# Optimization experiments

Measured on AMD Instinct MI355X. Metric: run time of the kernel, lower is better.

Reference implementation:

```python
import jax, jax.numpy as jnp
import numpy as np

N_QUBITS = 12          # log2(input_num)
DIM = 1 << N_QUBITS    # 4096
BATCH = 4096
OUTPUT_NUM = 10


def setup_inputs() -> dict:
    key = jax.random.key(0)
    k1, k2 = jax.random.split(key)
    x = jax.random.normal(k1, (BATCH, DIM), dtype=jnp.float32)
    # normalized statevectors (amplitude encoding), as a VQC expects
    x = x / jnp.linalg.norm(x, axis=1, keepdims=True)
    theta = jax.random.normal(k2, (2 * N_QUBITS,), dtype=jnp.float32) * jnp.pi
    return {"x": x, "theta": theta}


def _ry(theta):
    # [[cos(t/2), -sin(t/2)], [sin(t/2), cos(t/2)]]
    c, s = jnp.cos(theta / 2), jnp.sin(theta / 2)
    return jnp.stack([jnp.stack([c, -s]), jnp.stack([s, c])]).astype(jnp.complex64)


def _apply_1q(state, U, q, n):
    # state: [2^n, B]; qubit q is bit q of the row index (qubit 0 = LSB,
    # matching the kron ordering temp = kron(gate_i, temp) in the original).
    B = state.shape[1]
    hi = 1 << (n - 1 - q)
    lo = 1 << q
    s = state.reshape(hi, 2, lo * B)
    s = jnp.einsum('ab,xby->xay', U, s)
    return s.reshape(1 << n, B)


def _cz_phase(n):
    # vqc_10 applies CZ on adjacent pairs (n-2-i, n-1-i) for i in 0..n-2,
    # then CZ(0, n-1). CZ is diagonal; the swap sandwiches cancel exactly.
    idx = jnp.arange(1 << n)
    pairs = [(i, i + 1) for i in range(n - 1)] + [(0, n - 1)]
    par = jnp.zeros_like(idx)
    for p, q in pairs:
        par = par + ((idx >> p) & 1) * ((idx >> q) & 1)
    return jnp.where(par % 2 == 1, -1.0, 1.0).astype(jnp.complex64)


def reference(x, theta):
    n = N_QUBITS
    state = x.T.astype(jnp.complex64)            # [2^n, B]
    # first RY layer, thetas[0:n], theta[i] on qubit i
    for q in range(n):
        state = _apply_1q(state, _ry(theta[q]), q, n)
    # CZ entangling layer (diagonal)
    state = state * _cz_phase(n)[:, None]
    # second RY layer, thetas[n:2n]
    for q in range(n):
        state = _apply_1q(state, _ry(theta[n + q]), q, n)
    # measurement: P(qubit k == 1) for the first OUTPUT_NUM qubits
    probs = state.real ** 2 + state.imag ** 2    # [2^n, B]
    idx = jnp.arange(DIM)
    bits = ((idx[:, None] >> jnp.arange(OUTPUT_NUM)[None, :]) & 1).astype(probs.dtype)  # [2^n, K]
    out = jnp.einsum('db,dk->bk', probs, bits)   # [B, OUTPUT_NUM]
    return out
```

## Files before the change

kernel.cpp:

```cpp
#include <hip/hip_runtime.h>
#include <math.h>

#define DIM  4096
#define KOUT 10
#define BATCH 4096

typedef float float2v __attribute__((ext_vector_type(2)));

__device__ __forceinline__ int swzAddr(int lin) {
    return lin ^ (((lin >> 6) & 7) << 2);
}

__device__ __forceinline__ float rlane(float v, int lane) {
    return __int_as_float(__builtin_amdgcn_readlane(__float_as_int(v), lane));
}

__device__ __forceinline__ void ldsFence() {
    __builtin_amdgcn_sched_barrier(0);
    asm volatile("s_waitcnt lgkmcnt(0)" ::: "memory");
    __builtin_amdgcn_sched_barrier(0);
}

template<int KP>
__device__ __forceinline__ void liftPk(float2v r2[32], float t, float s) {
    const float2v tv = { -t, -t };
    const float2v sv = {  s,  s };
#pragma unroll
    for (int m = 0; m < 16; ++m) {
        const int i0 = ((m >> KP) << (KP + 1)) | (m & ((1 << KP) - 1));
        const int i1 = i0 | (1 << KP);
        float2v a = r2[i0], b = r2[i1];
        float2v a1 = __builtin_elementwise_fma(tv, b, a);
        float2v b1 = __builtin_elementwise_fma(sv, a1, b);
        r2[i1] = b1;
        r2[i0] = __builtin_elementwise_fma(tv, b1, a1);
    }
}

__device__ __forceinline__ void liftIntra(float2v r2[32], float t, float s) {
#pragma unroll
    for (int m = 0; m < 32; ++m) {
        float a = r2[m].x, b = r2[m].y;
        float a1 = fmaf(-t, b, a);
        float b1 = fmaf(s, a1, b);
        r2[m].x = fmaf(-t, b1, a1);
        r2[m].y = b1;
    }
}

__device__ __forceinline__ void transpose64(float2v r2[32], float* lds, int l) {
    float tmp[32];
    ldsFence();
    if (l < 32) {
#pragma unroll
        for (int e4 = 0; e4 < 16; ++e4)
            *reinterpret_cast<float4*>(&lds[swzAddr(l * 64 + e4 * 4)]) =
                make_float4(r2[2 * e4].x, r2[2 * e4].y,
                            r2[2 * e4 + 1].x, r2[2 * e4 + 1].y);
    }
#pragma unroll
    for (int j = 0; j < 32; ++j)
        tmp[j] = lds[swzAddr(j * 64 + l)];
    ldsFence();
    if (l >= 32) {
#pragma unroll
        for (int e4 = 0; e4 < 16; ++e4)
            *reinterpret_cast<float4*>(&lds[swzAddr((l - 32) * 64 + e4 * 4)]) =
                make_float4(r2[2 * e4].x, r2[2 * e4].y,
                            r2[2 * e4 + 1].x, r2[2 * e4 + 1].y);
    }
#pragma unroll
    for (int m = 0; m < 16; ++m) {
        float2v w;
        w.x = lds[swzAddr((2 * m) * 64 + l)];
        w.y = lds[swzAddr((2 * m + 1) * 64 + l)];
        r2[16 + m] = w;
    }
#pragma unroll
    for (int m = 0; m < 16; ++m) {
        float2v w; w.x = tmp[2 * m]; w.y = tmp[2 * m + 1];
        r2[m] = w;
    }
}

__global__ __launch_bounds__(64) void vqc_kernel(
        const float* __restrict__ x,
        const float* __restrict__ theta,
        float* __restrict__ out)
{
    __shared__ __align__(16) float lds[2048];
    const int l = threadIdx.x;
    const int b = blockIdx.x;

    float th = theta[l < 24 ? l : 0];
    float qh = 0.25f * th;
    float sq = sinf(qh), cq = cosf(qh);
    float sfull = 2.f * sq * cq;
    float tt, ss;
    if (fabsf(sq) <= fabsf(cq)) { tt = sq / cq;  ss = sfull;  }
    else                        { tt = -cq / sq; ss = -sfull; }

    float2v r2[32];
    const float4* x4 = reinterpret_cast<const float4*>(x + (size_t)b * DIM + l * 64);
#pragma unroll
    for (int e4 = 0; e4 < 16; ++e4) {
        const float4 w = x4[e4];
        float2v lo; lo.x = w.x; lo.y = w.y;
        float2v hi; hi.x = w.z; hi.y = w.w;
        r2[2 * e4]     = lo;
        r2[2 * e4 + 1] = hi;
    }

    liftIntra (r2, rlane(tt, 0), rlane(ss, 0));
    liftPk<0>(r2, rlane(tt, 1), rlane(ss, 1));
    liftPk<1>(r2, rlane(tt, 2), rlane(ss, 2));
    liftPk<2>(r2, rlane(tt, 3), rlane(ss, 3));
    liftPk<3>(r2, rlane(tt, 4), rlane(ss, 4));
    liftPk<4>(r2, rlane(tt, 5), rlane(ss, 5));

    transpose64(r2, lds, l);

    liftIntra (r2, rlane(tt, 6),  rlane(ss, 6));
    liftPk<0>(r2, rlane(tt, 7),  rlane(ss, 7));
    liftPk<1>(r2, rlane(tt, 8),  rlane(ss, 8));
    liftPk<2>(r2, rlane(tt, 9),  rlane(ss, 9));
    liftPk<3>(r2, rlane(tt, 10), rlane(ss, 10));
    liftPk<4>(r2, rlane(tt, 11), rlane(ss, 11));

    {
        int f  = __popc(l & (l >> 1) & 0x1F) & 1;
        int l5 = (l >> 5) & 1, l0 = l & 1;
        float sg0 = f              ? -1.f : 1.f;
        float sg1 = (f ^ l5)       ? -1.f : 1.f;
        float sg2 = (f ^ l0)       ? -1.f : 1.f;
        float sg3 = (f ^ l5 ^ l0)  ? -1.f : 1.f;
#pragma unroll
        for (int e = 0; e < 64; ++e) {
            const int Ce  = __popc(e & (e >> 1) & 0x1F) & 1;
            const int sel = (e & 1) | (((e >> 5) & 1) << 1);
            float sgn;
            if      (sel == 0) sgn = sg0;
            else if (sel == 1) sgn = sg1;
            else if (sel == 2) sgn = sg2;
            else               sgn = sg3;
            const float m = Ce ? -sgn : sgn;
            if (e & 1) r2[e >> 1].y *= m;
            else       r2[e >> 1].x *= m;
        }
    }

    liftIntra (r2, rlane(tt, 18), rlane(ss, 18));
    liftPk<0>(r2, rlane(tt, 19), rlane(ss, 19));
    liftPk<1>(r2, rlane(tt, 20), rlane(ss, 20));
    liftPk<2>(r2, rlane(tt, 21), rlane(ss, 21));
    liftPk<3>(r2, rlane(tt, 22), rlane(ss, 22));
    liftPk<4>(r2, rlane(tt, 23), rlane(ss, 23));

    transpose64(r2, lds, l);

    liftIntra (r2, rlane(tt, 12), rlane(ss, 12));
    liftPk<0>(r2, rlane(tt, 13), rlane(ss, 13));
    liftPk<1>(r2, rlane(tt, 14), rlane(ss, 14));
    liftPk<2>(r2, rlane(tt, 15), rlane(ss, 15));
    liftPk<3>(r2, rlane(tt, 16), rlane(ss, 16));
    liftPk<4>(r2, rlane(tt, 17), rlane(ss, 17));

#pragma unroll
    for (int m = 0; m < 32; ++m) r2[m] *= r2[m];

    float v0 = 0.f, v1 = 0.f, v2 = 0.f, v3 = 0.f, v4 = 0.f;
    float q32[32];
#pragma unroll
    for (int m = 0; m < 32; ++m) { v0 += r2[m].y; q32[m] = r2[m].x + r2[m].y; }
    float q16[16];
#pragma unroll
    for (int m = 0; m < 16; ++m) { v1 += q32[2*m+1]; q16[m] = q32[2*m] + q32[2*m+1]; }
    float q8[8];
#pragma unroll
    for (int m = 0; m < 8; ++m)  { v2 += q16[2*m+1]; q8[m] = q16[2*m] + q16[2*m+1]; }
    float q4[4];
#pragma unroll
    for (int m = 0; m < 4; ++m)  { v3 += q8[2*m+1]; q4[m] = q8[2*m] + q8[2*m+1]; }
    float q2[2];
#pragma unroll
    for (int m = 0; m < 2; ++m)  { v4 += q4[2*m+1]; q2[m] = q4[2*m] + q4[2*m+1]; }
    const float v5   = q2[1];
    const float psum = q2[0] + q2[1];

    float v[10];
    v[0] = v0; v[1] = v1; v[2] = v2; v[3] = v3; v[4] = v4; v[5] = v5;
    v[6] = (l & 1) ? psum : 0.f;
    v[7] = (l & 2) ? psum : 0.f;
    v[8] = (l & 4) ? psum : 0.f;
    v[9] = (l & 8) ? psum : 0.f;

#pragma unroll
    for (int k = 0; k < 10; ++k) {
        float t = v[k];
#pragma unroll
        for (int off = 32; off >= 1; off >>= 1)
            t += __shfl_xor(t, off, 64);
        v[k] = t;
    }

    if (l == 0) {
#pragma unroll
        for (int k = 0; k < KOUT; ++k) out[b * KOUT + k] = v[k];
    }
}

extern "C" void kernel_launch(void* const* d_in, const int* in_sizes, int n_in,
                              void* d_out, int out_size, void* d_ws, size_t ws_size,
                              hipStream_t stream) {
    const float* x     = (const float*)d_in[0];
    const float* theta = (const float*)d_in[1];
    float* out         = (float*)d_out;
    vqc_kernel<<<BATCH, 64, 0, stream>>>(x, theta, out);
}
```

Measured before the change: 27.31 us.

## Process two batch rows per wavefront to interleave independent work

Each 64-thread block now handles two statevectors (rows b and b+2048), interleaving their gate lifts, transposes and reductions so two independent dependency chains can hide each other's latency. The grid is halved to 2048 blocks, LDS per block doubles, and theta, sign and shuffle costs are amortised over two rows. In exchange, register use roughly doubles, which lowers occupancy or risks spills, and the smaller grid exposes fewer waves for latency hiding.

Result: slower. 31.99 us (+17.1%).

```diff
diff --git a/kernel.cpp b/kernel.cpp
--- a/kernel.cpp
+++ b/kernel.cpp
@@ -4,6 +4,7 @@
 #define DIM  4096
 #define KOUT 10
 #define BATCH 4096
+#define NBLK 2048
 
 typedef float float2v __attribute__((ext_vector_type(2)));
 
@@ -48,49 +49,83 @@
     }
 }
 
-__device__ __forceinline__ void transpose64(float2v r2[32], float* lds, int l) {
-    float tmp[32];
+__device__ __forceinline__ void writeRow(float* lds, int row, const float2v* r2) {
+#pragma unroll
+    for (int e4 = 0; e4 < 16; ++e4)
+        *reinterpret_cast<float4*>(&lds[swzAddr(row * 64 + e4 * 4)]) =
+            make_float4(r2[2 * e4].x, r2[2 * e4].y,
+                        r2[2 * e4 + 1].x, r2[2 * e4 + 1].y);
+}
+
+__device__ __forceinline__ void transposePair(float2v rA[32], float2v rB[32],
+                                              float* ldsA, float* ldsB, int l) {
+    float tA[32], tB[32];
     ldsFence();
-    if (l < 32) {
-#pragma unroll
-        for (int e4 = 0; e4 < 16; ++e4)
-            *reinterpret_cast<float4*>(&lds[swzAddr(l * 64 + e4 * 4)]) =
-                make_float4(r2[2 * e4].x, r2[2 * e4].y,
-                            r2[2 * e4 + 1].x, r2[2 * e4 + 1].y);
-    }
-#pragma unroll
-    for (int j = 0; j < 32; ++j)
-        tmp[j] = lds[swzAddr(j * 64 + l)];
+    if (l < 32) { writeRow(ldsA, l, rA); writeRow(ldsB, l, rB); }
+#pragma unroll
+    for (int j = 0; j < 32; ++j) tA[j] = ldsA[swzAddr(j * 64 + l)];
+#pragma unroll
+    for (int j = 0; j < 32; ++j) tB[j] = ldsB[swzAddr(j * 64 + l)];
     ldsFence();
-    if (l >= 32) {
-#pragma unroll
-        for (int e4 = 0; e4 < 16; ++e4)
-            *reinterpret_cast<float4*>(&lds[swzAddr((l - 32) * 64 + e4 * 4)]) =
-                make_float4(r2[2 * e4].x, r2[2 * e4].y,
-                            r2[2 * e4 + 1].x, r2[2 * e4 + 1].y);
-    }
+    if (l >= 32) { writeRow(ldsA, l - 32, rA); writeRow(ldsB, l - 32, rB); }
 #pragma unroll
     for (int m = 0; m < 16; ++m) {
         float2v w;
-        w.x = lds[swzAddr((2 * m) * 64 + l)];
-        w.y = lds[swzAddr((2 * m + 1) * 64 + l)];
-        r2[16 + m] = w;
+        w.x = ldsA[swzAddr((2 * m) * 64 + l)];
+        w.y = ldsA[swzAddr((2 * m + 1) * 64 + l)];
+        rA[16 + m] = w;
     }
 #pragma unroll
     for (int m = 0; m < 16; ++m) {
-        float2v w; w.x = tmp[2 * m]; w.y = tmp[2 * m + 1];
-        r2[m] = w;
-    }
-}
-
-__global__ __launch_bounds__(64) void vqc_kernel(
+        float2v w;
+        w.x = ldsB[swzAddr((2 * m) * 64 + l)];
+        w.y = ldsB[swzAddr((2 * m + 1) * 64 + l)];
+        rB[16 + m] = w;
+    }
+#pragma unroll
+    for (int m = 0; m < 16; ++m) { float2v w; w.x = tA[2*m]; w.y = tA[2*m+1]; rA[m] = w; }
+#pragma unroll
+    for (int m = 0; m < 16; ++m) { float2v w; w.x = tB[2*m]; w.y = tB[2*m+1]; rB[m] = w; }
+}
+
+__device__ __forceinline__ void measure(float2v r2[32], int l, float v[10]) {
+#pragma unroll
+    for (int m = 0; m < 32; ++m) r2[m] *= r2[m];
+    float v0 = 0.f, v1 = 0.f, v2 = 0.f, v3 = 0.f, v4 = 0.f;
+    float q32[32];
+#pragma unroll
+    for (int m = 0; m < 32; ++m) { v0 += r2[m].y; q32[m] = r2[m].x + r2[m].y; }
+    float q16[16];
+#pragma unroll
+    for (int m = 0; m < 16; ++m) { v1 += q32[2*m+1]; q16[m] = q32[2*m] + q32[2*m+1]; }
+    float q8[8];
+#pragma unroll
+    for (int m = 0; m < 8; ++m)  { v2 += q16[2*m+1]; q8[m] = q16[2*m] + q16[2*m+1]; }
+    float q4[4];
+#pragma unroll
+    for (int m = 0; m < 4; ++m)  { v3 += q8[2*m+1]; q4[m] = q8[2*m] + q8[2*m+1]; }
+    float q2[2];
+#pragma unroll
+    for (int m = 0; m < 2; ++m)  { v4 += q4[2*m+1]; q2[m] = q4[2*m] + q4[2*m+1]; }
+    const float v5   = q2[1];
+    const float psum = q2[0] + q2[1];
+    v[0] = v0; v[1] = v1; v[2] = v2; v[3] = v3; v[4] = v4; v[5] = v5;
+    v[6] = (l & 1) ? psum : 0.f;
+    v[7] = (l & 2) ? psum : 0.f;
+    v[8] = (l & 4) ? psum : 0.f;
+    v[9] = (l & 8) ? psum : 0.f;
+}
+
+__global__ __launch_bounds__(64, 2) void vqc_kernel(
         const float* __restrict__ x,
         const float* __restrict__ theta,
         float* __restrict__ out)
 {
-    __shared__ __align__(16) float lds[2048];
+    __shared__ __align__(16) float lds[2 * 2048];
     const int l = threadIdx.x;
     const int b = blockIdx.x;
+    float* ldsA = lds;
+    float* ldsB = lds + 2048;
 
     float th = theta[l < 24 ? l : 0];
     float qh = 0.25f * th;
@@ -100,32 +135,39 @@
     if (fabsf(sq) <= fabsf(cq)) { tt = sq / cq;  ss = sfull;  }
     else                        { tt = -cq / sq; ss = -sfull; }
 
-    float2v r2[32];
-    const float4* x4 = reinterpret_cast<const float4*>(x + (size_t)b * DIM + l * 64);
+    float2v rA[32], rB[32];
+    const float4* xA = reinterpret_cast<const float4*>(x + (size_t)b * DIM + l * 64);
+    const float4* xB = reinterpret_cast<const float4*>(x + (size_t)(b + NBLK) * DIM + l * 64);
 #pragma unroll
     for (int e4 = 0; e4 < 16; ++e4) {
-        const float4 w = x4[e4];
+        const float4 w = xA[e4];
         float2v lo; lo.x = w.x; lo.y = w.y;
         float2v hi; hi.x = w.z; hi.y = w.w;
-        r2[2 * e4]     = lo;
-        r2[2 * e4 + 1] = hi;
-    }
-
-    liftIntra (r2, rlane(tt, 0), rlane(ss, 0));
-    liftPk<0>(r2, rlane(tt, 1), rlane(ss, 1));
-    liftPk<1>(r2, rlane(tt, 2), rlane(ss, 2));
-    liftPk<2>(r2, rlane(tt, 3), rlane(ss, 3));
-    liftPk<3>(r2, rlane(tt, 4), rlane(ss, 4));
-    liftPk<4>(r2, rlane(tt, 5), rlane(ss, 5));
-
-    transpose64(r2, lds, l);
-
-    liftIntra (r2, rlane(tt, 6),  rlane(ss, 6));
-    liftPk<0>(r2, rlane(tt, 7),  rlane(ss, 7));
-    liftPk<1>(r2, rlane(tt, 8),  rlane(ss, 8));
-    liftPk<2>(r2, rlane(tt, 9),  rlane(ss, 9));
-    liftPk<3>(r2, rlane(tt, 10), rlane(ss, 10));
-    liftPk<4>(r2, rlane(tt, 11), rlane(ss, 11));
+        rA[2 * e4] = lo; rA[2 * e4 + 1] = hi;
+    }
+#pragma unroll
+    for (int e4 = 0; e4 < 16; ++e4) {
+        const float4 w = xB[e4];
+        float2v lo; lo.x = w.x; lo.y = w.y;
+        float2v hi; hi.x = w.z; hi.y = w.w;
+        rB[2 * e4] = lo; rB[2 * e4 + 1] = hi;
+    }
+
+    liftIntra (rA, rlane(tt, 0), rlane(ss, 0));  liftIntra (rB, rlane(tt, 0), rlane(ss, 0));
+    liftPk<0>(rA, rlane(tt, 1), rlane(ss, 1));   liftPk<0>(rB, rlane(tt, 1), rlane(ss, 1));
+    liftPk<1>(rA, rlane(tt, 2), rlane(ss, 2));   liftPk<1>(rB, rlane(tt, 2), rlane(ss, 2));
+    liftPk<2>(rA, rlane(tt, 3), rlane(ss, 3));   liftPk<2>(rB, rlane(tt, 3), rlane(ss, 3));
+    liftPk<3>(rA, rlane(tt, 4), rlane(ss, 4));   liftPk<3>(rB, rlane(tt, 4), rlane(ss, 4));
+    liftPk<4>(rA, rlane(tt, 5), rlane(ss, 5));   liftPk<4>(rB, rlane(tt, 5), rlane(ss, 5));
+
+    transposePair(rA, rB, ldsA, ldsB, l);
+
+    liftIntra (rA, rlane(tt, 6),  rlane(ss, 6));  liftIntra (rB, rlane(tt, 6),  rlane(ss, 6));
+    liftPk<0>(rA, rlane(tt, 7),  rlane(ss, 7));   liftPk<0>(rB, rlane(tt, 7),  rlane(ss, 7));
+    liftPk<1>(rA, rlane(tt, 8),  rlane(ss, 8));   liftPk<1>(rB, rlane(tt, 8),  rlane(ss, 8));
+    liftPk<2>(rA, rlane(tt, 9),  rlane(ss, 9));   liftPk<2>(rB, rlane(tt, 9),  rlane(ss, 9));
+    liftPk<3>(rA, rlane(tt, 10), rlane(ss, 10));  liftPk<3>(rB, rlane(tt, 10), rlane(ss, 10));
+    liftPk<4>(rA, rlane(tt, 11), rlane(ss, 11));  liftPk<4>(rB, rlane(tt, 11), rlane(ss, 11));
 
     {
         int f  = __popc(l & (l >> 1) & 0x1F) & 1;
@@ -144,68 +186,48 @@
             else if (sel == 2) sgn = sg2;
             else               sgn = sg3;
             const float m = Ce ? -sgn : sgn;
-            if (e & 1) r2[e >> 1].y *= m;
-            else       r2[e >> 1].x *= m;
+            if (e & 1) { rA[e >> 1].y *= m; rB[e >> 1].y *= m; }
+            else       { rA[e >> 1].x *= m; rB[e >> 1].x *= m; }
         }
     }
 
-    liftIntra (r2, rlane(tt, 18), rlane(ss, 18));
-    liftPk<0>(r2, rlane(tt, 19), rlane(ss, 19));
-    liftPk<1>(r2, rlane(tt, 20), rlane(ss, 20));
-    liftPk<2>(r2, rlane(tt, 21), rlane(ss, 21));
-    liftPk<3>(r2, rlane(tt, 22), rlane(ss, 22));
-    liftPk<4>(r2, rlane(tt, 23), rlane(ss, 23));
-
-    transpose64(r2, lds, l);
-
-    liftIntra (r2, rlane(tt, 12), rlane(ss, 12));
-    liftPk<0>(r2, rlane(tt, 13), rlane(ss, 13));
-    liftPk<1>(r2, rlane(tt, 14), rlane(ss, 14));
-    liftPk<2>(r2, rlane(tt, 15), rlane(ss, 15));
-    liftPk<3>(r2, rlane(tt, 16), rlane(ss, 16));
-    liftPk<4>(r2, rlane(tt, 17), rlane(ss, 17));
-
-#pragma unroll
-    for (int m = 0; m < 32; ++m) r2[m] *= r2[m];
-
-    float v0 = 0.f, v1 = 0.f, v2 = 0.f, v3 = 0.f, v4 = 0.f;
-    float q32[32];
-#pragma unroll
-    for (int m = 0; m < 32; ++m) { v0 += r2[m].y; q32[m] = r2[m].x + r2[m].y; }
-    float q16[16];
-#pragma unroll
-    for (int m = 0; m < 16; ++m) { v1 += q32[2*m+1]; q16[m] = q32[2*m] + q32[2*m+1]; }
-    float q8[8];
-#pragma unroll
-    for (int m = 0; m < 8; ++m)  { v2 += q16[2*m+1]; q8[m] = q16[2*m] + q16[2*m+1]; }
-    float q4[4];
-#pragma unroll
-    for (int m = 0; m < 4; ++m)  { v3 += q8[2*m+1]; q4[m] = q8[2*m] + q8[2*m+1]; }
-    float q2[2];
-#pragma unroll
-    for (int m = 0; m < 2; ++m)  { v4 += q4[2*m+1]; q2[m] = q4[2*m] + q4[2*m+1]; }
-    const float v5   = q2[1];
-    const float psum = q2[0] + q2[1];
-
-    float v[10];
-    v[0] = v0; v[1] = v1; v[2] = v2; v[3] = v3; v[4] = v4; v[5] = v5;
-    v[6] = (l & 1) ? psum : 0.f;
-    v[7] = (l & 2) ? psum : 0.f;
-    v[8] = (l & 4) ? psum : 0.f;
-    v[9] = (l & 8) ? psum : 0.f;
-
-#pragma unroll
-    for (int k = 0; k < 10; ++k) {
-        float t = v[k];
-#pragma unroll
-        for (int off = 32; off >= 1; off >>= 1)
-            t += __shfl_xor(t, off, 64);
-        v[k] = t;
+    liftIntra (rA, rlane(tt, 18), rlane(ss, 18)); liftIntra (rB, rlane(tt, 18), rlane(ss, 18));
+    liftPk<0>(rA, rlane(tt, 19), rlane(ss, 19));  liftPk<0>(rB, rlane(tt, 19), rlane(ss, 19));
+    liftPk<1>(rA, rlane(tt, 20), rlane(ss, 20));  liftPk<1>(rB, rlane(tt, 20), rlane(ss, 20));
+    liftPk<2>(rA, rlane(tt, 21), rlane(ss, 21));  liftPk<2>(rB, rlane(tt, 21), rlane(ss, 21));
+    liftPk<3>(rA, rlane(tt, 22), rlane(ss, 22));  liftPk<3>(rB, rlane(tt, 22), rlane(ss, 22));
+    liftPk<4>(rA, rlane(tt, 23), rlane(ss, 23));  liftPk<4>(rB, rlane(tt, 23), rlane(ss, 23));
+
+    transposePair(rA, rB, ldsA, ldsB, l);
+
+    liftIntra (rA, rlane(tt, 12), rlane(ss, 12)); liftIntra (rB, rlane(tt, 12), rlane(ss, 12));
+    liftPk<0>(rA, rlane(tt, 13), rlane(ss, 13));  liftPk<0>(rB, rlane(tt, 13), rlane(ss, 13));
+    liftPk<1>(rA, rlane(tt, 14), rlane(ss, 14));  liftPk<1>(rB, rlane(tt, 14), rlane(ss, 14));
+    liftPk<2>(rA, rlane(tt, 15), rlane(ss, 15));  liftPk<2>(rB, rlane(tt, 15), rlane(ss, 15));
+    liftPk<3>(rA, rlane(tt, 16), rlane(ss, 16));  liftPk<3>(rB, rlane(tt, 16), rlane(ss, 16));
+    liftPk<4>(rA, rlane(tt, 17), rlane(ss, 17));  liftPk<4>(rB, rlane(tt, 17), rlane(ss, 17));
+
+    float vA[10], vB[10];
+    measure(rA, l, vA);
+    measure(rB, l, vB);
+
+#pragma unroll
+    for (int k = 0; k < KOUT; ++k) {
+        float ta = vA[k], tb = vB[k];
+#pragma unroll
+        for (int off = 32; off >= 1; off >>= 1) {
+            ta += __shfl_xor(ta, off, 64);
+            tb += __shfl_xor(tb, off, 64);
+        }
+        vA[k] = ta; vB[k] = tb;
     }
 
     if (l == 0) {
 #pragma unroll
-        for (int k = 0; k < KOUT; ++k) out[b * KOUT + k] = v[k];
+        for (int k = 0; k < KOUT; ++k) {
+            out[b * KOUT + k]          = vA[k];
+            out[(b + NBLK) * KOUT + k] = vB[k];
+        }
     }
 }
 
@@ -215,5 +237,5 @@
     const float* x     = (const float*)d_in[0];
     const float* theta = (const float*)d_in[1];
     float* out         = (float*)d_out;
-    vqc_kernel<<<BATCH, 64, 0, stream>>>(x, theta, out);
-}
+    vqc_kernel<<<NBLK, 64, 0, stream>>>(x, theta, out);
+}
```
